# Optimization experiments

Measured on AMD Instinct MI355X. Metric: run time of the kernel, lower is better.

## Reference

```python
import jax, jax.numpy as jnp
import numpy as np

N_NODES = 100000
N_EDGES = 1600000
FDIM = 128


def setup_inputs() -> dict:
    key = jax.random.key(0)
    k1, k2 = jax.random.split(key)
    x = jax.random.normal(k1, (N_NODES, FDIM), dtype=jnp.float32)
    edge_index = jax.random.randint(k2, (2, N_EDGES), 0, N_NODES, dtype=jnp.int64)
    # GCNConv params as loaded by the module: identity weight, zero bias
    W = jnp.eye(FDIM, dtype=jnp.float32)
    bias = jnp.zeros((FDIM,), dtype=jnp.float32)
    return {"x": x, "W": W, "bias": bias, "edge_index": edge_index}


def reference(x, W, bias, edge_index):
    n = x.shape[0]
    src, dst = edge_index[0], edge_index[1]
    # GCNConv default: add self-loops with weight 1.0
    loop = jnp.arange(n, dtype=edge_index.dtype)
    src_f = jnp.concatenate([src, loop])
    dst_f = jnp.concatenate([dst, loop])
    ew = jnp.ones(src_f.shape[0], dtype=x.dtype)
    # symmetric normalization: deg computed on destination (col)
    deg = jax.ops.segment_sum(ew, dst_f, num_segments=n)
    dinv = jnp.where(deg > 0, deg ** -0.5, 0.0).astype(x.dtype)
    norm = dinv[src_f] * dinv[dst_f]  # [E+n]
    h = x @ W.T  # linear transform (W = I here, but kept faithful)
    msg = h[src_f] * norm[:, None]  # gather + scale, [E+n, fdim]
    out = jax.ops.segment_sum(msg, dst_f, num_segments=n) + bias  # scatter-add
    return jnp.sum(out, axis=0, keepdims=True)  # [1, fdim]
```

## Files before the change

### kernel.cpp

```cpp
#include <hip/hip_runtime.h>

#define FD 128
#define CHD 32768
#define NSLD 64
#define CHS 16384
#define NSLS 32
#define RXB 512
#define QSCALE 16777216.0f
#define QINV   5.9604644775390625e-8f
#define QS14   16384.0f
#define QI14   6.103515625e-5f
#define SRCMASK 0x1FFFFu

__device__ __forceinline__ unsigned quant_w(int dp1) {
    return (unsigned)(rsqrtf((float)dp1) * QSCALE + 0.5f);
}
__device__ __forceinline__ unsigned quant_w14(int dp1) {
    return (unsigned)(rsqrtf((float)dp1) * QS14 + 0.5f);
}

__device__ __forceinline__ bool detect_is32_wave(const unsigned int* w, long long nwords) {
    const int lane = threadIdx.x & 63;
    const long long i0 = 2 * lane + 1, i1 = 2 * (lane + 64) + 1;
    unsigned acc = 0;
    if (i0 < nwords) acc |= w[i0];
    if (i1 < nwords) acc |= w[i1];
    return __ballot(acc != 0u) != 0ull;
}

__device__ __forceinline__ int4 ld_e4(const void* ei, bool is32, long long off, long long i) {
    if (is32) return *reinterpret_cast<const int4*>((const int*)ei + off + i);
    const long long* p = (const long long*)ei + off + i;
    longlong2 a = *reinterpret_cast<const longlong2*>(p);
    longlong2 b = *reinterpret_cast<const longlong2*>(p + 2);
    return make_int4((int)a.x, (int)a.y, (int)b.x, (int)b.y);
}
__device__ __forceinline__ int ld_e1(const void* ei, bool is32, long long idx) {
    return is32 ? ((const int*)ei)[idx] : (int)((const long long*)ei)[idx];
}

__global__ __launch_bounds__(512) void hist_deg_kernel(
        const void* __restrict__ ei, unsigned int* __restrict__ psD,
        long long E, long long SL, int nch) {
    __shared__ unsigned int hist[CHD / 2];
    const int tid = threadIdx.x;
    const bool is32 = detect_is32_wave((const unsigned int*)ei, 2 * E);
    const int b = blockIdx.x, c = b % nch, j = b / nch;
    const int lo = c * CHD;
    for (int i = tid; i < CHD / 2; i += 512) hist[i] = 0u;
    __syncthreads();
    const long long e0 = (long long)j * SL;
    long long e1 = e0 + SL; if (e1 > E) e1 = E; if (e1 < e0) e1 = e0;
    const long long e1v = e0 + ((e1 - e0) & ~3LL);
    for (long long i = e0 + (long long)tid * 4; i < e1v; i += 2048) {
        int4 d = ld_e4(ei, is32, E, i);
        unsigned u0 = (unsigned)(d.x - lo), u1 = (unsigned)(d.y - lo);
        unsigned u2 = (unsigned)(d.z - lo), u3 = (unsigned)(d.w - lo);
        if (u0 < CHD) atomicAdd(&hist[u0 >> 1], 1u << ((u0 & 1) * 16));
        if (u1 < CHD) atomicAdd(&hist[u1 >> 1], 1u << ((u1 & 1) * 16));
        if (u2 < CHD) atomicAdd(&hist[u2 >> 1], 1u << ((u2 & 1) * 16));
        if (u3 < CHD) atomicAdd(&hist[u3 >> 1], 1u << ((u3 & 1) * 16));
    }
    { long long it = e1v + tid;
      if (it < e1) { unsigned u = (unsigned)(ld_e1(ei, is32, E + it) - lo);
                     if (u < CHD) atomicAdd(&hist[u >> 1], 1u << ((u & 1) * 16)); } }
    __syncthreads();
    unsigned int* o = psD + (size_t)b * (CHD / 2);
    for (int w = tid; w < CHD / 2; w += 512) o[w] = hist[w];
}

__global__ void deg_reduce_kernel(const unsigned int* __restrict__ psD,
                                  int* __restrict__ deg, long long n, int nch) {
    const long long tw = blockIdx.x * (long long)blockDim.x + threadIdx.x;
    if (tw >= (long long)nch * (CHD / 2)) return;
    const int cc = (int)(tw / (CHD / 2));
    const int w  = (int)(tw % (CHD / 2));
    unsigned s0 = 0, s1 = 0;
    for (int j = 0; j < NSLD; ++j) {
        unsigned v = psD[((size_t)j * nch + cc) * (CHD / 2) + w];
        s0 += v & 0xffffu; s1 += v >> 16;
    }
    const long long v0 = (long long)cc * CHD + 2 * w;
    if (v0 < n) deg[v0] = (int)s0;
    if (v0 + 1 < n) deg[v0 + 1] = (int)s1;
}

__global__ __launch_bounds__(256) void qwpack_kernel(
        const void* __restrict__ ei, const int* __restrict__ deg,
        unsigned int* __restrict__ qp, long long E) {
    const bool is32 = detect_is32_wave((const unsigned int*)ei, 2 * E);
    const long long stride4 = (long long)gridDim.x * blockDim.x * 4;
    const long long E4 = E & ~3LL;
    for (long long i = (blockIdx.x * (long long)blockDim.x + threadIdx.x) * 4;
         i < E4; i += stride4) {
        int4 s = ld_e4(ei, is32, 0, i);
        int4 d = ld_e4(ei, is32, E, i);
        uint4 q;
        q.x = (quant_w14(deg[d.x] + 1) << 17) | (unsigned)s.x;
        q.y = (quant_w14(deg[d.y] + 1) << 17) | (unsigned)s.y;
        q.z = (quant_w14(deg[d.z] + 1) << 17) | (unsigned)s.z;
        q.w = (quant_w14(deg[d.w] + 1) << 17) | (unsigned)s.w;
        *reinterpret_cast<uint4*>(qp + i) = q;
    }
    const long long st1 = (long long)gridDim.x * blockDim.x;
    for (long long k = E4 + blockIdx.x * (long long)blockDim.x + threadIdx.x;
         k < E; k += st1)
        qp[k] = (quant_w14(deg[ld_e1(ei, is32, E + k)] + 1) << 17) |
                (unsigned)ld_e1(ei, is32, k);
}

__global__ __launch_bounds__(512) void hist_s_kernel(
        const unsigned int* __restrict__ qp, unsigned int* __restrict__ psS,
        long long E, long long SL, int nch) {
    __shared__ unsigned int hist[CHS];
    const int tid = threadIdx.x;
    const int b = blockIdx.x, c = b % nch, j = b / nch;
    const int lo = c * CHS;
    for (int i = tid; i < CHS; i += 512) hist[i] = 0u;
    __syncthreads();
    const long long e0 = (long long)j * SL;
    long long e1 = e0 + SL; if (e1 > E) e1 = E; if (e1 < e0) e1 = e0;
    const long long e1v = e0 + ((e1 - e0) & ~3LL);
    for (long long i = e0 + (long long)tid * 4; i < e1v; i += 2048) {
        uint4 p = *reinterpret_cast<const uint4*>(qp + i);
        unsigned u0 = (p.x & SRCMASK) - lo, u1 = (p.y & SRCMASK) - lo;
        unsigned u2 = (p.z & SRCMASK) - lo, u3 = (p.w & SRCMASK) - lo;
        if (u0 < CHS) atomicAdd(&hist[u0], p.x >> 17);
        if (u1 < CHS) atomicAdd(&hist[u1], p.y >> 17);
        if (u2 < CHS) atomicAdd(&hist[u2], p.z >> 17);
        if (u3 < CHS) atomicAdd(&hist[u3], p.w >> 17);
    }
    { long long it = e1v + tid;
      if (it < e1) { unsigned p = qp[it];
                     unsigned u = (p & SRCMASK) - lo;
                     if (u < CHS) atomicAdd(&hist[u], p >> 17); } }
    __syncthreads();
    unsigned int* o = psS + (size_t)b * CHS;
    for (int w = tid; w < CHS; w += 512) o[w] = hist[w];
}

__global__ __launch_bounds__(256) void reduce_x_coef_kernel(
        const float* __restrict__ x, const int* __restrict__ deg,
        const unsigned int* __restrict__ psS, float* __restrict__ P,
        long long n, int nch) {
    __shared__ float lcoef[1024];
    __shared__ float4 sm4[256];
    const int tid = threadIdx.x;
    const long long vlo = (long long)blockIdx.x * n / RXB;
    const long long vhi = ((long long)blockIdx.x + 1) * n / RXB;
    const int nv = (int)(vhi - vlo);
    for (int t = tid; t < nv; t += 256) {
        const long long v = vlo + t;
        const int cc = (int)(v / CHS);
        const int u  = (int)(v % CHS);
        unsigned s = 0;
        #pragma unroll 8
        for (int jj = 0; jj < NSLS; ++jj)
            s += psS[((size_t)jj * nch + cc) * CHS + u];
        const float dg = (float)(deg[v] + 1);
        const float di = rsqrtf(dg);
        lcoef[t] = di * ((float)s * QI14) + 1.0f / dg;
    }
    __syncthreads();
    float4 a = make_float4(0.f, 0.f, 0.f, 0.f);
    const long long i0 = vlo * (FD / 4), i1 = vhi * (FD / 4);
    for (long long i = i0 + tid; i < i1; i += 256) {
        const float cf = lcoef[(int)((i >> 5) - vlo)];
        const float4 xv = reinterpret_cast<const float4*>(x)[i];
        a.x += cf * xv.x; a.y += cf * xv.y; a.z += cf * xv.z; a.w += cf * xv.w;
    }
    const int lane = tid & 31, grp = tid >> 5;
    sm4[grp * 32 + lane] = a;
    __syncthreads();
    for (int s2 = 4; s2 > 0; s2 >>= 1) {
        if (grp < s2) {
            float4 o = sm4[(grp + s2) * 32 + lane];
            float4 m = sm4[grp * 32 + lane];
            m.x += o.x; m.y += o.y; m.z += o.z; m.w += o.w;
            sm4[grp * 32 + lane] = m;
        }
        __syncthreads();
    }
    if (tid < 32) reinterpret_cast<float4*>(P)[blockIdx.x * 32 + tid] = sm4[tid];
}

__global__ __launch_bounds__(256) void colsum_final_kernel(
        const float* __restrict__ P, const float* __restrict__ Wm,
        const float* __restrict__ bias, float* __restrict__ out, float nn) {
    __shared__ float wrow[FD];
    __shared__ float red[256];
    const int f = blockIdx.x, tid = threadIdx.x;
    if (tid < FD) wrow[tid] = Wm[f * FD + tid];
    __syncthreads();
    float part = 0.f;
    for (int j = tid; j < RXB; j += 256) {
        const float4* Pj = reinterpret_cast<const float4*>(P + (size_t)j * FD);
        #pragma unroll
        for (int k = 0; k < FD / 4; ++k) {
            float4 p = Pj[k];
            part += wrow[4 * k] * p.x + wrow[4 * k + 1] * p.y +
                    wrow[4 * k + 2] * p.z + wrow[4 * k + 3] * p.w;
        }
    }
    red[tid] = part;
    __syncthreads();
    for (int s2 = 128; s2 > 0; s2 >>= 1) {
        if (tid < s2) red[tid] += red[tid + s2];
        __syncthreads();
    }
    if (tid == 0) out[f] = red[0] + nn * bias[f];
}

__global__ void deg_fb(const void* __restrict__ ei, int* __restrict__ deg, long long E) {
    const bool is32 = detect_is32_wave((const unsigned int*)ei, 2 * E);
    const long long st = (long long)gridDim.x * blockDim.x;
    long long i = blockIdx.x * (long long)blockDim.x + threadIdx.x;
    for (; i < E; i += st) atomicAdd(&deg[ld_e1(ei, is32, E + i)], 1);
}

__global__ void srcsum_fb(const void* __restrict__ ei, const int* __restrict__ deg,
                          unsigned int* __restrict__ Sq, long long E) {
    const bool is32 = detect_is32_wave((const unsigned int*)ei, 2 * E);
    const long long st = (long long)gridDim.x * blockDim.x;
    long long i = blockIdx.x * (long long)blockDim.x + threadIdx.x;
    for (; i < E; i += st)
        atomicAdd(&Sq[ld_e1(ei, is32, i)], quant_w(deg[ld_e1(ei, is32, E + i)] + 1));
}

__global__ void coef_fb(unsigned int* __restrict__ Sq, const int* __restrict__ deg,
                        long long n) {
    const long long v = blockIdx.x * (long long)blockDim.x + threadIdx.x;
    if (v >= n) return;
    unsigned s = Sq[v];
    float dg = (float)(deg[v] + 1);
    float di = rsqrtf(dg);
    ((float*)Sq)[v] = di * ((float)s * QINV) + 1.0f / dg;
}

__global__ void redx_fb(const float* __restrict__ x, const float* __restrict__ coef,
                        float* __restrict__ t, long long n) {
    __shared__ float sm[FD];
    for (int f = threadIdx.x; f < FD; f += blockDim.x) sm[f] = 0.f;
    __syncthreads();
    const long long tot = n * (FD / 4);
    const long long st = (long long)gridDim.x * blockDim.x;
    const int lane = threadIdx.x & 31;
    float4 a = make_float4(0.f, 0.f, 0.f, 0.f);
    for (long long i = blockIdx.x * (long long)blockDim.x + threadIdx.x; i < tot; i += st) {
        float cf = coef[i >> 5];
        float4 xv = reinterpret_cast<const float4*>(x)[i];
        a.x += cf * xv.x; a.y += cf * xv.y; a.z += cf * xv.z; a.w += cf * xv.w;
    }
    atomicAdd(&sm[lane * 4 + 0], a.x);
    atomicAdd(&sm[lane * 4 + 1], a.y);
    atomicAdd(&sm[lane * 4 + 2], a.z);
    atomicAdd(&sm[lane * 4 + 3], a.w);
    __syncthreads();
    for (int f = threadIdx.x; f < FD; f += blockDim.x) atomicAdd(&t[f], sm[f]);
}

__global__ void final_fb(const float* __restrict__ Wm, const float* __restrict__ bias,
                         const float* __restrict__ t, float* __restrict__ out, float nn) {
    __shared__ float ts[FD];
    int f = threadIdx.x;
    if (f < FD) ts[f] = t[f];
    __syncthreads();
    if (f < FD) {
        float a0 = 0.f;
        #pragma unroll 16
        for (int k = 0; k < FD; ++k) a0 += Wm[f * FD + k] * ts[k];
        out[f] = a0 + nn * bias[f];
    }
}

extern "C" void kernel_launch(void* const* d_in, const int* in_sizes, int n_in,
                              void* d_out, int out_size, void* d_ws, size_t ws_size,
                              hipStream_t stream) {
    const float* x    = (const float*)d_in[0];
    const float* W    = (const float*)d_in[1];
    const float* bias = (const float*)d_in[2];
    const void*  ei   = d_in[3];
    float* out = (float*)d_out;
    const long long n = in_sizes[0] / FD;
    const long long E = (long long)in_sizes[3] / 2;

    const int NCHD = (int)((n + CHD - 1) / CHD);
    const int NCHS = (int)((n + CHS - 1) / CHS);
    const long long SLD = ((E + NSLD - 1) / NSLD + 3) & ~3LL;
    const long long SLS = ((E + NSLS - 1) / NSLS + 3) & ~3LL;

    char* ws = (char*)d_ws;
    size_t off = 0;
    auto take = [&](size_t bytes) { size_t r = off; off += (bytes + 255) & ~(size_t)255; return r; };
    unsigned int* psD = (unsigned int*)(ws + take((size_t)NCHD * NSLD * (CHD / 2) * 4));
    unsigned int* psS = (unsigned int*)(ws + take((size_t)NCHS * NSLS * CHS * 4));
    int*          deg = (int*)(ws + take((size_t)n * 4));
    unsigned int* qp  = (unsigned int*)(ws + take((size_t)E * 4));
    float*        P   = (float*)(ws + take((size_t)RXB * FD * 4));
    const size_t need = off;

    const bool main_ok = (ws_size >= need) && ((E & 3) == 0) && (E >= 512) &&
                         (SLD < 65536) && (n <= (1LL << 17)) &&
                         (n <= (long long)RXB * 1024);

    if (main_ok) {
        hist_deg_kernel<<<NCHD * NSLD, 512, 0, stream>>>(ei, psD, E, SLD, NCHD);
        {
            long long nw = (long long)NCHD * (CHD / 2);
            deg_reduce_kernel<<<(int)((nw + 255) / 256), 256, 0, stream>>>(psD, deg, n, NCHD);
        }
        qwpack_kernel<<<1024, 256, 0, stream>>>(ei, deg, qp, E);
        hist_s_kernel<<<NCHS * NSLS, 512, 0, stream>>>(qp, psS, E, SLS, NCHS);
        reduce_x_coef_kernel<<<RXB, 256, 0, stream>>>(x, deg, psS, P, n, NCHS);
        colsum_final_kernel<<<FD, 256, 0, stream>>>(P, W, bias, out, (float)n);
    } else {
        int*          degF = (int*)ws;
        unsigned int* Sq   = (unsigned int*)(ws + (size_t)n * 4);
        float*        tF   = (float*)(ws + (size_t)n * 8);
        hipMemsetAsync(ws, 0, (size_t)n * 8 + 512, stream);
        deg_fb<<<1600, 256, 0, stream>>>(ei, degF, E);
        srcsum_fb<<<1600, 256, 0, stream>>>(ei, degF, Sq, E);
        coef_fb<<<(int)((n + 255) / 256), 256, 0, stream>>>(Sq, degF, n);
        redx_fb<<<2048, 256, 0, stream>>>(x, (const float*)Sq, tF, n);
        final_fb<<<1, FD, 0, stream>>>(W, bias, tF, out, (float)n);
    }
}
```

Before: 73.27 us.

## Partition packed edges by source chunk and pack degree histogram into bytes

The qwpack stage now buckets packed (weight, src) words by source chunk into per-chunk global partitions, using shared-memory staging buffers and global atomic counters. The hist_s kernel then reads only its own chunk's partition instead of scanning every edge and discarding out-of-range ones. Separately, the degree histogram packs four 8-bit counters per word so a chunk of 65536 nodes fits in shared memory, halving the number of degree-pass blocks. The costs are heavy block-level synchronisation and a larger workspace in the pack kernel, and 8-bit counters can overflow if a slice gives one node more than 255 in-edges.

```diff
diff --git a/kernel.cpp b/kernel.cpp
--- a/kernel.cpp
+++ b/kernel.cpp
@@ -1,10 +1,12 @@
 #include <hip/hip_runtime.h>
 
 #define FD 128
-#define CHD 32768
+#define CHD 65536
 #define NSLD 64
 #define CHS 16384
-#define NSLS 32
+#define LOG2CHS 14
+#define NSLS 16
+#define QPB 512
 #define RXB 512
 #define QSCALE 16777216.0f
 #define QINV   5.9604644775390625e-8f
@@ -41,13 +43,14 @@
 
 __global__ __launch_bounds__(512) void hist_deg_kernel(
         const void* __restrict__ ei, unsigned int* __restrict__ psD,
-        long long E, long long SL, int nch) {
-    __shared__ unsigned int hist[CHD / 2];
+        unsigned int* __restrict__ counts, long long E, long long SL, int nch) {
+    __shared__ unsigned int hist[CHD / 4];
     const int tid = threadIdx.x;
+    if (blockIdx.x == 0 && tid < 16) counts[tid] = 0u;
     const bool is32 = detect_is32_wave((const unsigned int*)ei, 2 * E);
     const int b = blockIdx.x, c = b % nch, j = b / nch;
     const int lo = c * CHD;
-    for (int i = tid; i < CHD / 2; i += 512) hist[i] = 0u;
+    for (int i = tid; i < CHD / 4; i += 512) hist[i] = 0u;
     __syncthreads();
     const long long e0 = (long long)j * SL;
     long long e1 = e0 + SL; if (e1 > E) e1 = E; if (e1 < e0) e1 = e0;
@@ -56,84 +59,112 @@
         int4 d = ld_e4(ei, is32, E, i);
         unsigned u0 = (unsigned)(d.x - lo), u1 = (unsigned)(d.y - lo);
         unsigned u2 = (unsigned)(d.z - lo), u3 = (unsigned)(d.w - lo);
-        if (u0 < CHD) atomicAdd(&hist[u0 >> 1], 1u << ((u0 & 1) * 16));
-        if (u1 < CHD) atomicAdd(&hist[u1 >> 1], 1u << ((u1 & 1) * 16));
-        if (u2 < CHD) atomicAdd(&hist[u2 >> 1], 1u << ((u2 & 1) * 16));
-        if (u3 < CHD) atomicAdd(&hist[u3 >> 1], 1u << ((u3 & 1) * 16));
+        if (u0 < CHD) atomicAdd(&hist[u0 >> 2], 1u << ((u0 & 3) * 8));
+        if (u1 < CHD) atomicAdd(&hist[u1 >> 2], 1u << ((u1 & 3) * 8));
+        if (u2 < CHD) atomicAdd(&hist[u2 >> 2], 1u << ((u2 & 3) * 8));
+        if (u3 < CHD) atomicAdd(&hist[u3 >> 2], 1u << ((u3 & 3) * 8));
     }
     { long long it = e1v + tid;
       if (it < e1) { unsigned u = (unsigned)(ld_e1(ei, is32, E + it) - lo);
-                     if (u < CHD) atomicAdd(&hist[u >> 1], 1u << ((u & 1) * 16)); } }
-    __syncthreads();
-    unsigned int* o = psD + (size_t)b * (CHD / 2);
-    for (int w = tid; w < CHD / 2; w += 512) o[w] = hist[w];
+                     if (u < CHD) atomicAdd(&hist[u >> 2], 1u << ((u & 3) * 8)); } }
+    __syncthreads();
+    unsigned int* o = psD + (size_t)b * (CHD / 4);
+    for (int w = tid; w < CHD / 4; w += 512) o[w] = hist[w];
 }
 
 __global__ void deg_reduce_kernel(const unsigned int* __restrict__ psD,
                                   int* __restrict__ deg, long long n, int nch) {
     const long long tw = blockIdx.x * (long long)blockDim.x + threadIdx.x;
-    if (tw >= (long long)nch * (CHD / 2)) return;
-    const int cc = (int)(tw / (CHD / 2));
-    const int w  = (int)(tw % (CHD / 2));
-    unsigned s0 = 0, s1 = 0;
+    if (tw >= (long long)nch * (CHD / 4)) return;
+    const int cc = (int)(tw / (CHD / 4));
+    const int w  = (int)(tw % (CHD / 4));
+    unsigned s0 = 0, s1 = 0, s2 = 0, s3 = 0;
     for (int j = 0; j < NSLD; ++j) {
-        unsigned v = psD[((size_t)j * nch + cc) * (CHD / 2) + w];
-        s0 += v & 0xffffu; s1 += v >> 16;
-    }
-    const long long v0 = (long long)cc * CHD + 2 * w;
-    if (v0 < n) deg[v0] = (int)s0;
+        unsigned v = psD[((size_t)j * nch + cc) * (CHD / 4) + w];
+        s0 += v & 0xFFu; s1 += (v >> 8) & 0xFFu;
+        s2 += (v >> 16) & 0xFFu; s3 += v >> 24;
+    }
+    const long long v0 = (long long)cc * CHD + 4 * w;
+    if (v0 < n)     deg[v0]     = (int)s0;
     if (v0 + 1 < n) deg[v0 + 1] = (int)s1;
-}
-
-__global__ __launch_bounds__(256) void qwpack_kernel(
+    if (v0 + 2 < n) deg[v0 + 2] = (int)s2;
+    if (v0 + 3 < n) deg[v0 + 3] = (int)s3;
+}
+
+__global__ __launch_bounds__(512) void qwpack_part_kernel(
         const void* __restrict__ ei, const int* __restrict__ deg,
-        unsigned int* __restrict__ qp, long long E) {
+        unsigned int* __restrict__ counts, unsigned int* __restrict__ qpart,
+        long long capC, long long E, int nch) {
+    __shared__ unsigned int buf[8][1024];
+    __shared__ int cnt[8], take[8], base[8];
+    const int tid = threadIdx.x;
     const bool is32 = detect_is32_wave((const unsigned int*)ei, 2 * E);
-    const long long stride4 = (long long)gridDim.x * blockDim.x * 4;
-    const long long E4 = E & ~3LL;
-    for (long long i = (blockIdx.x * (long long)blockDim.x + threadIdx.x) * 4;
-         i < E4; i += stride4) {
-        int4 s = ld_e4(ei, is32, 0, i);
-        int4 d = ld_e4(ei, is32, E, i);
-        uint4 q;
-        q.x = (quant_w14(deg[d.x] + 1) << 17) | (unsigned)s.x;
-        q.y = (quant_w14(deg[d.y] + 1) << 17) | (unsigned)s.y;
-        q.z = (quant_w14(deg[d.z] + 1) << 17) | (unsigned)s.z;
-        q.w = (quant_w14(deg[d.w] + 1) << 17) | (unsigned)s.w;
-        *reinterpret_cast<uint4*>(qp + i) = q;
-    }
-    const long long st1 = (long long)gridDim.x * blockDim.x;
-    for (long long k = E4 + blockIdx.x * (long long)blockDim.x + threadIdx.x;
-         k < E; k += st1)
-        qp[k] = (quant_w14(deg[ld_e1(ei, is32, E + k)] + 1) << 17) |
-                (unsigned)ld_e1(ei, is32, k);
+    if (tid < 8) cnt[tid] = 0;
+    __syncthreads();
+    const long long e0 = (long long)blockIdx.x * E / QPB;
+    const long long e1 = (long long)(blockIdx.x + 1) * E / QPB;
+    for (long long s = e0; s < e1; s += 512) {
+        const long long idx = s + tid;
+        if (idx < e1) {
+            const int src = ld_e1(ei, is32, idx);
+            const int dst = ld_e1(ei, is32, E + idx);
+            const unsigned p = (quant_w14(deg[dst] + 1) << 17) | (unsigned)src;
+            const int c = src >> LOG2CHS;
+            const int pos = atomicAdd(&cnt[c], 1);
+            buf[c][pos] = p;
+        }
+        __syncthreads();
+        if (tid < 8) {
+            const int k = cnt[tid] & ~511;
+            take[tid] = k;
+            if (k) base[tid] = (int)atomicAdd(&counts[tid], (unsigned)k);
+        }
+        __syncthreads();
+        for (int c = 0; c < nch; ++c) {
+            const int k = take[c];
+            if (k) {
+                unsigned int* dp = qpart + (size_t)c * capC + base[c];
+                for (int t = tid; t < k; t += 512) dp[t] = buf[c][t];
+            }
+        }
+        __syncthreads();
+        for (int c = 0; c < nch; ++c) {
+            const int k = take[c], r = cnt[c] - k;
+            if (k && r > 0)
+                for (int t = tid; t < r; t += 512) buf[c][t] = buf[c][k + t];
+        }
+        __syncthreads();
+        if (tid < 8) cnt[tid] -= take[tid];
+        __syncthreads();
+    }
+    if (tid < 8) { take[tid] = cnt[tid];
+                   if (cnt[tid]) base[tid] = (int)atomicAdd(&counts[tid], (unsigned)cnt[tid]); }
+    __syncthreads();
+    for (int c = 0; c < nch; ++c) {
+        const int k = take[c];
+        if (k) {
+            unsigned int* dp = qpart + (size_t)c * capC + base[c];
+            for (int t = tid; t < k; t += 512) dp[t] = buf[c][t];
+        }
+    }
 }
 
 __global__ __launch_bounds__(512) void hist_s_kernel(
-        const unsigned int* __restrict__ qp, unsigned int* __restrict__ psS,
-        long long E, long long SL, int nch) {
+        const unsigned int* __restrict__ qpart, const unsigned int* __restrict__ counts,
+        unsigned int* __restrict__ psS, long long capC, int nch) {
     __shared__ unsigned int hist[CHS];
     const int tid = threadIdx.x;
     const int b = blockIdx.x, c = b % nch, j = b / nch;
     const int lo = c * CHS;
     for (int i = tid; i < CHS; i += 512) hist[i] = 0u;
     __syncthreads();
-    const long long e0 = (long long)j * SL;
-    long long e1 = e0 + SL; if (e1 > E) e1 = E; if (e1 < e0) e1 = e0;
-    const long long e1v = e0 + ((e1 - e0) & ~3LL);
-    for (long long i = e0 + (long long)tid * 4; i < e1v; i += 2048) {
-        uint4 p = *reinterpret_cast<const uint4*>(qp + i);
-        unsigned u0 = (p.x & SRCMASK) - lo, u1 = (p.y & SRCMASK) - lo;
-        unsigned u2 = (p.z & SRCMASK) - lo, u3 = (p.w & SRCMASK) - lo;
-        if (u0 < CHS) atomicAdd(&hist[u0], p.x >> 17);
-        if (u1 < CHS) atomicAdd(&hist[u1], p.y >> 17);
-        if (u2 < CHS) atomicAdd(&hist[u2], p.z >> 17);
-        if (u3 < CHS) atomicAdd(&hist[u3], p.w >> 17);
-    }
-    { long long it = e1v + tid;
-      if (it < e1) { unsigned p = qp[it];
-                     unsigned u = (p & SRCMASK) - lo;
-                     if (u < CHS) atomicAdd(&hist[u], p >> 17); } }
+    const long long cc = counts[c];
+    const long long i0 = cc * j / NSLS, i1 = cc * (j + 1) / NSLS;
+    const unsigned int* src = qpart + (size_t)c * capC;
+    for (long long i = i0 + tid; i < i1; i += 512) {
+        const unsigned p = src[i];
+        atomicAdd(&hist[(p & SRCMASK) - lo], p >> 17);
+    }
     __syncthreads();
     unsigned int* o = psS + (size_t)b * CHS;
     for (int w = tid; w < CHS; w += 512) o[w] = hist[w];
@@ -151,10 +182,10 @@
     const int nv = (int)(vhi - vlo);
     for (int t = tid; t < nv; t += 256) {
         const long long v = vlo + t;
-        const int cc = (int)(v / CHS);
-        const int u  = (int)(v % CHS);
+        const int cc = (int)(v >> LOG2CHS);
+        const int u  = (int)(v & (CHS - 1));
         unsigned s = 0;
-        #pragma unroll 8
+        #pragma unroll
         for (int jj = 0; jj < NSLS; ++jj)
             s += psS[((size_t)jj * nch + cc) * CHS + u];
         const float dg = (float)(deg[v] + 1);
@@ -287,30 +318,31 @@
     const int NCHD = (int)((n + CHD - 1) / CHD);
     const int NCHS = (int)((n + CHS - 1) / CHS);
     const long long SLD = ((E + NSLD - 1) / NSLD + 3) & ~3LL;
-    const long long SLS = ((E + NSLS - 1) / NSLS + 3) & ~3LL;
+    const long long capC = (E + 255) & ~255LL;
 
     char* ws = (char*)d_ws;
     size_t off = 0;
     auto take = [&](size_t bytes) { size_t r = off; off += (bytes + 255) & ~(size_t)255; return r; };
-    unsigned int* psD = (unsigned int*)(ws + take((size_t)NCHD * NSLD * (CHD / 2) * 4));
-    unsigned int* psS = (unsigned int*)(ws + take((size_t)NCHS * NSLS * CHS * 4));
-    int*          deg = (int*)(ws + take((size_t)n * 4));
-    unsigned int* qp  = (unsigned int*)(ws + take((size_t)E * 4));
-    float*        P   = (float*)(ws + take((size_t)RXB * FD * 4));
+    unsigned int* psD    = (unsigned int*)(ws + take((size_t)NCHD * NSLD * (CHD / 4) * 4));
+    unsigned int* psS    = (unsigned int*)(ws + take((size_t)NCHS * NSLS * CHS * 4));
+    int*          deg    = (int*)(ws + take((size_t)n * 4));
+    unsigned int* qpart  = (unsigned int*)(ws + take((size_t)NCHS * capC * 4));
+    unsigned int* counts = (unsigned int*)(ws + take(256));
+    float*        P      = (float*)(ws + take((size_t)RXB * FD * 4));
     const size_t need = off;
 
     const bool main_ok = (ws_size >= need) && ((E & 3) == 0) && (E >= 512) &&
-                         (SLD < 65536) && (n <= (1LL << 17)) &&
+                         (n <= (1LL << 17)) && (NCHS <= 8) &&
                          (n <= (long long)RXB * 1024);
 
     if (main_ok) {
-        hist_deg_kernel<<<NCHD * NSLD, 512, 0, stream>>>(ei, psD, E, SLD, NCHD);
+        hist_deg_kernel<<<NCHD * NSLD, 512, 0, stream>>>(ei, psD, counts, E, SLD, NCHD);
         {
-            long long nw = (long long)NCHD * (CHD / 2);
+            long long nw = (long long)NCHD * (CHD / 4);
             deg_reduce_kernel<<<(int)((nw + 255) / 256), 256, 0, stream>>>(psD, deg, n, NCHD);
         }
-        qwpack_kernel<<<1024, 256, 0, stream>>>(ei, deg, qp, E);
-        hist_s_kernel<<<NCHS * NSLS, 512, 0, stream>>>(qp, psS, E, SLS, NCHS);
+        qwpack_part_kernel<<<QPB, 512, 0, stream>>>(ei, deg, counts, qpart, capC, E, NCHS);
+        hist_s_kernel<<<NCHS * NSLS, 512, 0, stream>>>(qpart, counts, psS, capC, NCHS);
         reduce_x_coef_kernel<<<RXB, 256, 0, stream>>>(x, deg, psS, P, n, NCHS);
         colsum_final_kernel<<<FD, 256, 0, stream>>>(P, W, bias, out, (float)n);
     } else {
```

After: 89.84 us. 1.23x slower.
